# Kernel tuning notes

Measured on AMD Instinct MI355X. Metric: run time of the kernel, lower is better.

The kernel has to match this reference:

```python
import jax, jax.numpy as jnp
import numpy as np

TEMP = 0.07      # InfoNCE temperature
NB = 15          # neighborhood side length
HALF = NB // 2
NUM_SAMPLES = 256
EPS = 1e-8       # F.cosine_similarity eps


def setup_inputs() -> dict:
    key = jax.random.key(0)
    k1, k2, k3, k4 = jax.random.split(key, 4)
    B, D, H, W = 8, 128, 256, 256
    features = jax.random.normal(k1, (B, D, H, W), jnp.float32)
    targets = jax.random.randint(k2, (B, H, W), 0, 4, jnp.int32)
    # anchors restricted to the valid interior [HALF, H-HALF)
    anchor_h = jax.random.randint(k3, (B, NUM_SAMPLES), HALF, H - HALF, jnp.int32)
    anchor_w = jax.random.randint(k4, (B, NUM_SAMPLES), HALF, W - HALF, jnp.int32)
    return {"features": features, "targets": targets,
            "anchor_h": anchor_h, "anchor_w": anchor_w}


def _local_contrastive_loss(features, targets, anchor_h, anchor_w):
    offs = jnp.arange(-HALF, HALF + 1)  # (NB,)

    def per_image(feat, lab, ah, aw):
        # feat: (D,H,W), lab: (H,W), ah/aw: (N,)
        N = ah.shape[0]
        wh = jnp.broadcast_to(ah[:, None, None] + offs[None, :, None], (N, NB, NB))
        ww = jnp.broadcast_to(aw[:, None, None] + offs[None, None, :], (N, NB, NB))
        patch = feat[:, wh, ww]          # (D, N, NB, NB) gathered local windows
        plab = lab[wh, ww]               # (N, NB, NB)
        af = feat[:, ah, aw]             # (D, N) anchor features
        alab = lab[ah, aw]               # (N,)
        # cosine similarity (with eps clamp like F.cosine_similarity), / temperature
        an = jnp.maximum(jnp.sqrt(jnp.sum(af * af, axis=0)), EPS)          # (N,)
        pn = jnp.maximum(jnp.sqrt(jnp.sum(patch * patch, axis=0)), EPS)    # (N,NB,NB)
        sim = jnp.einsum('dn,dnkl->nkl', af, patch) / (an[:, None, None] * pn) / TEMP
        # positive mask: same label, centre pixel excluded
        pos = plab == alab[:, None, None]
        pos = pos.at[:, HALF, HALF].set(False)
        sim_flat = sim.reshape(N, -1)                 # (N, NB*NB)
        pos_flat = pos.reshape(N, -1)
        pos_cnt = pos_flat.sum(-1)                    # (N,)
        lse = jax.nn.logsumexp(sim_flat, axis=-1)     # (N,)
        pos_mean = jnp.where(pos_flat, sim_flat, 0.0).sum(-1) / jnp.maximum(pos_cnt, 1)
        valid = pos_cnt > 0
        loss_i = -(pos_mean - lse)
        return jnp.where(valid, loss_i, 0.0).sum(), valid.sum()

    losses, counts = jax.vmap(per_image)(features, targets, anchor_h, anchor_w)
    total = losses.sum()
    cnt = counts.sum()
    return jnp.where(cnt > 0,
                     total / jnp.maximum(cnt, 1).astype(total.dtype),
                     jnp.zeros((), total.dtype))


def reference(features, targets, anchor_h, anchor_w):
    return _local_contrastive_loss(features, targets, anchor_h, anchor_w)
```

## Files before the change

### kernel.cpp

```cpp
#include <hip/hip_runtime.h>
#include <math.h>

#define TEMPC   0.07f
#define NBK     15
#define HALFK   7
#define NPOS    225
#define DD      128
#define HHH     256
#define WWW     256
#define PLANE   (HHH * WWW)
#define EPSC    1e-8f

__global__ __launch_bounds__(256) void lcl_main(
    const float* __restrict__ feat,
    const int*   __restrict__ targ,
    const int*   __restrict__ anch_h,
    const int*   __restrict__ anch_w,
    float*       __restrict__ loss_part,
    float*       __restrict__ cnt_part)
{
    const int bn   = blockIdx.x;
    const int b    = bn >> 8;
    const int tid  = threadIdx.x;
    const int lane = tid & 63;
    const int wave = tid >> 6;

    __shared__ float af[DD];
    __shared__ float red[4], red2[4], red3[4];
    __shared__ float s_an;
    __shared__ float s_max;

    const int ah = anch_h[bn];
    const int aw = anch_w[bn];
    const int* lab = targ + b * PLANE;
    const int alab = lab[ah * WWW + aw];
    const float* fb = feat + (size_t)b * DD * PLANE;

    float sqa = 0.f;
    if (tid < DD) {
        float v = fb[(size_t)tid * PLANE + ah * WWW + aw];
        af[tid] = v;
        sqa = v * v;
    }
    #pragma unroll
    for (int off = 32; off; off >>= 1) sqa += __shfl_down(sqa, off, 64);
    if (lane == 0) red[wave] = sqa;
    __syncthreads();
    if (tid == 0) s_an = fmaxf(sqrtf(red[0] + red[1] + red[2] + red[3]), EPSC);
    __syncthreads();
    const float an = s_an;

    const bool active = tid < NPOS;
    float dot = 0.f, sq = 0.f;
    int hh = 0, ww = 0;
    if (active) {
        const int k = tid / NBK;
        const int l = tid - k * NBK;
        hh = ah - HALFK + k;
        ww = aw - HALFK + l;
        const float* p = fb + hh * WWW + ww;
        #pragma unroll 16
        for (int d = 0; d < DD; ++d) {
            float v = p[d * PLANE];
            dot = fmaf(af[d], v, dot);
            sq  = fmaf(v,     v, sq);
        }
    }

    float sim = -INFINITY;
    bool  pos = false;
    if (active) {
        float pn = fmaxf(sqrtf(sq), EPSC);
        sim = dot / (an * pn * TEMPC);
        pos = (lab[hh * WWW + ww] == alab) && (tid != (HALFK * NBK + HALFK));
    }

    float m = sim;
    #pragma unroll
    for (int off = 32; off; off >>= 1) m = fmaxf(m, __shfl_down(m, off, 64));
    if (lane == 0) red[wave] = m;
    __syncthreads();
    if (tid == 0) s_max = fmaxf(fmaxf(red[0], red[1]), fmaxf(red[2], red[3]));
    __syncthreads();
    m = s_max;

    float e  = active ? expf(sim - m) : 0.f;
    float ps = pos ? sim : 0.f;
    float pc = pos ? 1.f : 0.f;
    #pragma unroll
    for (int off = 32; off; off >>= 1) {
        e  += __shfl_down(e,  off, 64);
        ps += __shfl_down(ps, off, 64);
        pc += __shfl_down(pc, off, 64);
    }
    if (lane == 0) { red[wave] = e; red2[wave] = ps; red3[wave] = pc; }
    __syncthreads();
    if (tid == 0) {
        float E  = red[0]  + red[1]  + red[2]  + red[3];
        float PS = red2[0] + red2[1] + red2[2] + red2[3];
        float PC = red3[0] + red3[1] + red3[2] + red3[3];
        float lse = m + logf(E);
        bool valid = PC > 0.5f;
        loss_part[bn] = valid ? (lse - PS / PC) : 0.f;
        cnt_part[bn]  = valid ? 1.f : 0.f;
    }
}

__global__ __launch_bounds__(256) void lcl_finalize(
    const float* __restrict__ loss_part,
    const float* __restrict__ cnt_part,
    float*       __restrict__ out,
    int n)
{
    const int tid  = threadIdx.x;
    const int lane = tid & 63;
    const int wave = tid >> 6;
    __shared__ float rs[4], rc[4];

    float s = 0.f, c = 0.f;
    for (int i = tid; i < n; i += 256) {
        s += loss_part[i];
        c += cnt_part[i];
    }
    #pragma unroll
    for (int off = 32; off; off >>= 1) {
        s += __shfl_down(s, off, 64);
        c += __shfl_down(c, off, 64);
    }
    if (lane == 0) { rs[wave] = s; rc[wave] = c; }
    __syncthreads();
    if (tid == 0) {
        float S = rs[0] + rs[1] + rs[2] + rs[3];
        float C = rc[0] + rc[1] + rc[2] + rc[3];
        out[0] = (C > 0.5f) ? (S / C) : 0.f;
    }
}

extern "C" void kernel_launch(void* const* d_in, const int* in_sizes, int n_in,
                              void* d_out, int out_size, void* d_ws, size_t ws_size,
                              hipStream_t stream) {
    const float* feat  = (const float*)d_in[0];
    const int*   targ  = (const int*)d_in[1];
    const int*   anchh = (const int*)d_in[2];
    const int*   anchw = (const int*)d_in[3];
    float* out = (float*)d_out;

    const int n_anchors = in_sizes[2];

    float* loss_part = (float*)d_ws;
    float* cnt_part  = loss_part + n_anchors;

    lcl_main<<<n_anchors, 256, 0, stream>>>(feat, targ, anchh, anchw,
                                            loss_part, cnt_part);
    lcl_finalize<<<1, 256, 0, stream>>>(loss_part, cnt_part, out, n_anchors);
}
```

Before: 378.0 us.

## Restructure into row sweep with per-row anchor dot accumulation and precomputed norms

Replaces the per-anchor gather kernel with three stages. One kernel gathers anchor features, and one kernel streams each image row once, coalesced, through shared memory. That row kernel computes pixel norms for the whole image and accumulates dot products for every anchor whose window covers the row. A final per-anchor kernel does the softmax. The goal is to remove the strided, uncoalesced 128-channel gathers that reload overlapping windows many times. In exchange the code reads the full feature tensor once, adds workspace traffic and extra launches, and depends on the anchor count per image being 256.

Result: no change. 378.1 us (+0.0%).

```diff
diff --git a/kernel.cpp b/kernel.cpp
--- a/kernel.cpp
+++ b/kernel.cpp
@@ -9,13 +9,133 @@
 #define HHH     256
 #define WWW     256
 #define PLANE   (HHH * WWW)
+#define NSAMP   256
 #define EPSC    1e-8f
 
-__global__ __launch_bounds__(256) void lcl_main(
+#define CCH     32
+#define NCH     (DD / CCH)
+#define GRP     16
+#define MAXA    256
+#define MAXP    (MAXA * NBK)
+
+__global__ __launch_bounds__(256) void k_afgather(
     const float* __restrict__ feat,
+    const int*   __restrict__ anch_h,
+    const int*   __restrict__ anch_w,
+    float*       __restrict__ afg,
+    int n_anchors)
+{
+    int idx = blockIdx.x * 256 + threadIdx.x;
+    if (idx >= n_anchors * DD) return;
+    int bn = idx >> 7;
+    int d  = idx & 127;
+    int b  = bn >> 8;
+    int ah = anch_h[bn], aw = anch_w[bn];
+    afg[idx] = feat[(size_t)b * DD * PLANE + d * PLANE + ah * WWW + aw];
+}
+
+__global__ __launch_bounds__(256) void k_sweep(
+    const float* __restrict__ feat,
+    const int*   __restrict__ anch_h,
+    const int*   __restrict__ anch_w,
+    const float* __restrict__ afg,
+    float*       __restrict__ dot_out,
+    float*       __restrict__ normimg)
+{
+    const int bh   = blockIdx.x;
+    const int b    = bh >> 8;
+    const int h    = bh & 255;
+    const int tid  = threadIdx.x;
+    const int lane = tid & 63;
+    const int wave = tid >> 6;
+
+    __shared__ float rows[CCH][WWW];
+    __shared__ float dacc[MAXP];
+    __shared__ float afl[GRP][33];
+    __shared__ int   s_n[MAXA], s_aw[MAXA], s_k[MAXA];
+    __shared__ int   wcnt[4];
+
+    const int ah_t = anch_h[b * NSAMP + tid];
+    const bool in  = (ah_t - h <= HALFK) && (h - ah_t <= HALFK);
+    unsigned long long m = __ballot(in);
+    if (lane == 0) wcnt[wave] = __popcll(m);
+    __syncthreads();
+    const int ncnt = wcnt[0] + wcnt[1] + wcnt[2] + wcnt[3];
+    if (in) {
+        int base = 0;
+        #pragma unroll
+        for (int w = 0; w < 4; ++w) if (w < wave) base += wcnt[w];
+        int p = base + __popcll(m & ((1ULL << lane) - 1ULL));
+        s_n[p]  = tid;
+        s_aw[p] = anch_w[b * NSAMP + tid];
+        s_k[p]  = h - ah_t + HALFK;
+    }
+    __syncthreads();
+    if (ncnt == 0) return;
+
+    const int npos = ncnt * NBK;
+    for (int p = tid; p < npos; p += 256) dacc[p] = 0.f;
+
+    const float* fbh = feat + (size_t)b * DD * PLANE + h * WWW;
+    const int ngrp = (ncnt + GRP - 1) / GRP;
+    float nrm = 0.f;
+
+    for (int c = 0; c < NCH; ++c) {
+        const int ch0 = c * CCH;
+        __syncthreads();
+        #pragma unroll
+        for (int i = 0; i < 8; ++i) {
+            int f  = i * 256 + tid;
+            int ch = f >> 6;
+            int c4 = f & 63;
+            *(float4*)&rows[ch][c4 * 4] =
+                *(const float4*)&fbh[(size_t)(ch0 + ch) * PLANE + c4 * 4];
+        }
+        __syncthreads();
+        #pragma unroll
+        for (int ch = 0; ch < CCH; ++ch) {
+            float v = rows[ch][tid];
+            nrm = fmaf(v, v, nrm);
+        }
+        for (int g = 0; g < ngrp; ++g) {
+            const int a0 = g * GRP;
+            const int na = min(GRP, ncnt - a0);
+            __syncthreads();
+            for (int f = tid; f < na * CCH; f += 256) {
+                int j = f >> 5, cc = f & 31;
+                afl[j][cc] = afg[(size_t)(b * NSAMP + s_n[a0 + j]) * DD + ch0 + cc];
+            }
+            __syncthreads();
+            const int np = na * NBK;
+            if (tid < np) {
+                int j    = tid / NBK;
+                int cpos = tid - j * NBK;
+                int col  = s_aw[a0 + j] - HALFK + cpos;
+                float dsum = 0.f;
+                #pragma unroll
+                for (int ch = 0; ch < CCH; ++ch)
+                    dsum = fmaf(afl[j][ch], rows[ch][col], dsum);
+                dacc[a0 * NBK + tid] += dsum;
+            }
+        }
+    }
+
+    normimg[(b * HHH + h) * WWW + tid] = nrm;
+    __syncthreads();
+    for (int p = tid; p < npos; p += 256) {
+        int slot = p / NBK;
+        int cpos = p - slot * NBK;
+        int bn   = b * NSAMP + s_n[slot];
+        dot_out[bn * NPOS + s_k[slot] * NBK + cpos] = dacc[p];
+    }
+}
+
+__global__ __launch_bounds__(256) void k_softmax(
     const int*   __restrict__ targ,
     const int*   __restrict__ anch_h,
     const int*   __restrict__ anch_w,
+    const float* __restrict__ dot_out,
+    const float* __restrict__ normimg,
     float*       __restrict__ loss_part,
     float*       __restrict__ cnt_part)
 {
@@ -24,67 +144,36 @@
     const int tid  = threadIdx.x;
     const int lane = tid & 63;
     const int wave = tid >> 6;
-
-    __shared__ float af[DD];
     __shared__ float red[4], red2[4], red3[4];
-    __shared__ float s_an;
     __shared__ float s_max;
 
-    const int ah = anch_h[bn];
-    const int aw = anch_w[bn];
+    const int ah = anch_h[bn], aw = anch_w[bn];
     const int* lab = targ + b * PLANE;
     const int alab = lab[ah * WWW + aw];
-    const float* fb = feat + (size_t)b * DD * PLANE;
-
-    float sqa = 0.f;
-    if (tid < DD) {
-        float v = fb[(size_t)tid * PLANE + ah * WWW + aw];
-        af[tid] = v;
-        sqa = v * v;
-    }
-    #pragma unroll
-    for (int off = 32; off; off >>= 1) sqa += __shfl_down(sqa, off, 64);
-    if (lane == 0) red[wave] = sqa;
-    __syncthreads();
-    if (tid == 0) s_an = fmaxf(sqrtf(red[0] + red[1] + red[2] + red[3]), EPSC);
-    __syncthreads();
-    const float an = s_an;
+    const float an = fmaxf(sqrtf(normimg[(b * HHH + ah) * WWW + aw]), EPSC);
 
     const bool active = tid < NPOS;
-    float dot = 0.f, sq = 0.f;
-    int hh = 0, ww = 0;
-    if (active) {
-        const int k = tid / NBK;
-        const int l = tid - k * NBK;
-        hh = ah - HALFK + k;
-        ww = aw - HALFK + l;
-        const float* p = fb + hh * WWW + ww;
-        #pragma unroll 16
-        for (int d = 0; d < DD; ++d) {
-            float v = p[d * PLANE];
-            dot = fmaf(af[d], v, dot);
-            sq  = fmaf(v,     v, sq);
-        }
-    }
-
     float sim = -INFINITY;
     bool  pos = false;
     if (active) {
-        float pn = fmaxf(sqrtf(sq), EPSC);
+        int k  = tid / NBK, l = tid - (tid / NBK) * NBK;
+        int hh = ah - HALFK + k, ww = aw - HALFK + l;
+        float dot = dot_out[bn * NPOS + tid];
+        float pn  = fmaxf(sqrtf(normimg[(b * HHH + hh) * WWW + ww]), EPSC);
         sim = dot / (an * pn * TEMPC);
         pos = (lab[hh * WWW + ww] == alab) && (tid != (HALFK * NBK + HALFK));
     }
 
-    float m = sim;
+    float mx = sim;
     #pragma unroll
-    for (int off = 32; off; off >>= 1) m = fmaxf(m, __shfl_down(m, off, 64));
-    if (lane == 0) red[wave] = m;
+    for (int off = 32; off; off >>= 1) mx = fmaxf(mx, __shfl_down(mx, off, 64));
+    if (lane == 0) red[wave] = mx;
     __syncthreads();
     if (tid == 0) s_max = fmaxf(fmaxf(red[0], red[1]), fmaxf(red[2], red[3]));
     __syncthreads();
-    m = s_max;
-
-    float e  = active ? expf(sim - m) : 0.f;
+    mx = s_max;
+
+    float e  = active ? expf(sim - mx) : 0.f;
     float ps = pos ? sim : 0.f;
     float pc = pos ? 1.f : 0.f;
     #pragma unroll
@@ -99,7 +188,7 @@
         float E  = red[0]  + red[1]  + red[2]  + red[3];
         float PS = red2[0] + red2[1] + red2[2] + red2[3];
         float PC = red3[0] + red3[1] + red3[2] + red3[3];
-        float lse = m + logf(E);
+        float lse = mx + logf(E);
         bool valid = PC > 0.5f;
         loss_part[bn] = valid ? (lse - PS / PC) : 0.f;
         cnt_part[bn]  = valid ? 1.f : 0.f;
@@ -146,11 +235,19 @@
     float* out = (float*)d_out;
 
     const int n_anchors = in_sizes[2];
-
-    float* loss_part = (float*)d_ws;
+    const int B = n_anchors / NSAMP;
+
+    float* afg       = (float*)d_ws;
+    float* dot_out   = afg      + (size_t)n_anchors * DD;
+    float* normimg   = dot_out  + (size_t)n_anchors * NPOS;
+    float* loss_part = normimg  + (size_t)B * PLANE;
     float* cnt_part  = loss_part + n_anchors;
 
-    lcl_main<<<n_anchors, 256, 0, stream>>>(feat, targ, anchh, anchw,
-                                            loss_part, cnt_part);
+    k_afgather<<<(n_anchors * DD + 255) / 256, 256, 0, stream>>>(
+        feat, anchh, anchw, afg, n_anchors);
+    k_sweep<<<B * HHH, 256, 0, stream>>>(
+        feat, anchh, anchw, afg, dot_out, normimg);
+    k_softmax<<<n_anchors, 256, 0, stream>>>(
+        targ, anchh, anchw, dot_out, normimg, loss_part, cnt_part);
     lcl_finalize<<<1, 256, 0, stream>>>(loss_part, cnt_part, out, n_anchors);
 }
```
